# Optimization experiments

Measured on AMD Instinct MI355X. Metric: run time of the kernel, lower is better.

## Reference

```python
import jax, jax.numpy as jnp
import numpy as np

E = 800000
N_NODES = 25000
NUM_RADIAL = 6
HIDDEN = 256
OUT_EMB = 256
OUT_CH = 1
NUM_LAYERS = 3


def setup_inputs() -> dict:
    key = jax.random.key(0)
    ks = jax.random.split(key, 10)
    s = lambda fan_in: 1.0 / np.sqrt(fan_in)
    return {
        "x": jax.random.normal(ks[0], (E, HIDDEN), dtype=jnp.float32),
        "rbf": jax.random.normal(ks[1], (E, NUM_RADIAL), dtype=jnp.float32),
        "i": jax.random.randint(ks[2], (E,), 0, N_NODES, dtype=jnp.int64),
        "num_nodes": N_NODES,
        "W_rbf": jax.random.normal(ks[3], (HIDDEN, NUM_RADIAL), dtype=jnp.float32) * s(NUM_RADIAL),
        "W_up": jax.random.normal(ks[4], (OUT_EMB, HIDDEN), dtype=jnp.float32) * s(HIDDEN),
        "b_up": jnp.zeros((OUT_EMB,), dtype=jnp.float32),
        "Ws": jax.random.normal(ks[5], (NUM_LAYERS, OUT_EMB, OUT_EMB), dtype=jnp.float32) * s(OUT_EMB),
        "bs": jnp.zeros((NUM_LAYERS, OUT_EMB), dtype=jnp.float32),
        "W_out": jax.random.normal(ks[6], (OUT_CH, OUT_EMB), dtype=jnp.float32) * s(OUT_EMB),
    }


def reference(x, rbf, i, num_nodes, W_rbf, W_up, b_up, Ws, bs, W_out):
    # edge-wise: lin_rbf(rbf) * x  -> [E, hidden]
    h = jnp.einsum("er,hr->eh", rbf, W_rbf) * x
    # scatter-sum edges to nodes -> [N, hidden]
    h = jax.ops.segment_sum(h, i, num_segments=num_nodes)
    # lin_up (with bias) -> [N, out_emb]
    h = jnp.einsum("nh,oh->no", h, W_up) + b_up
    # MLP stack with swish activation
    for l in range(Ws.shape[0]):
        h = jax.nn.silu(jnp.einsum("no,po->np", h, Ws[l]) + bs[l])
    # final linear, no bias -> [N, out_channels]
    return jnp.einsum("no,co->nc", h, W_out)
```

## Files before the change

### kernel.cpp

```cpp
#include <hip/hip_runtime.h>
#include <stddef.h>

#define E_EDGES   800000
#define N_NODES   25000
#define NRADIAL   6
#define HIDDEN    256
#define OUT_EMB   256
#define NUM_LAYERS 3

__global__ void count_kernel(const int* __restrict__ idx, int* __restrict__ cnt) {
    int e = blockIdx.x * blockDim.x + threadIdx.x;
    if (e < E_EDGES) atomicAdd(&cnt[idx[e]], 1);
}

__global__ __launch_bounds__(1024) void scan_kernel(const int* __restrict__ cnt,
                                                    int* __restrict__ off,
                                                    int* __restrict__ cur) {
    __shared__ int warpsum[16];
    const int PER = 25;
    int t = threadIdx.x;
    int base = t * PER;
    int local[PER];
    int s = 0;
    #pragma unroll
    for (int j = 0; j < PER; ++j) {
        int n = base + j;
        int v = (n < N_NODES) ? cnt[n] : 0;
        local[j] = s;
        s += v;
    }
    int lane = t & 63, w = t >> 6;
    int incl = s;
    #pragma unroll
    for (int d = 1; d < 64; d <<= 1) {
        int y = __shfl_up(incl, d, 64);
        if (lane >= d) incl += y;
    }
    if (lane == 63) warpsum[w] = incl;
    __syncthreads();
    if (w == 0) {
        int v = (lane < 16) ? warpsum[lane] : 0;
        #pragma unroll
        for (int d = 1; d < 16; d <<= 1) {
            int y = __shfl_up(v, d, 64);
            if (lane >= d) v += y;
        }
        if (lane < 16) warpsum[lane] = v;
    }
    __syncthreads();
    int wbase = (w > 0) ? warpsum[w - 1] : 0;
    int texcl = wbase + (incl - s);
    #pragma unroll
    for (int j = 0; j < PER; ++j) {
        int n = base + j;
        if (n < N_NODES) { int o = texcl + local[j]; off[n] = o; cur[n] = o; }
    }
}

__global__ void fill_kernel(const int* __restrict__ idx, int* __restrict__ cur,
                            int* __restrict__ elist) {
    int e = blockIdx.x * blockDim.x + threadIdx.x;
    if (e < E_EDGES) {
        int n = idx[e];
        int pos = atomicAdd(&cur[n], 1);
        elist[pos] = e;
    }
}

__global__ __launch_bounds__(256) void gather_kernel(
        const float* __restrict__ x, const float* __restrict__ rbf,
        const float* __restrict__ W_rbf,
        const int* __restrict__ off, const int* __restrict__ cnt,
        const int* __restrict__ elist, float* __restrict__ node_h) {
    int wave = threadIdx.x >> 6;
    int lane = threadIdx.x & 63;
    int node = blockIdx.x * 4 + wave;
    if (node >= N_NODES) return;
    int c0 = lane * 4;

    float wr[4][NRADIAL];
    #pragma unroll
    for (int j = 0; j < 4; ++j)
        #pragma unroll
        for (int r = 0; r < NRADIAL; ++r)
            wr[j][r] = W_rbf[(c0 + j) * NRADIAL + r];

    float a0 = 0.f, a1 = 0.f, a2 = 0.f, a3 = 0.f;
    int start = off[node];
    int ne    = cnt[node];
    #pragma unroll 2
    for (int k = 0; k < ne; ++k) {
        int e = elist[start + k];
        const float2* r2 = reinterpret_cast<const float2*>(rbf + (size_t)e * NRADIAL);
        float2 ra = r2[0], rb = r2[1], rc = r2[2];
        float r0 = ra.x, r1 = ra.y, r2v = rb.x, r3 = rb.y, r4 = rc.x, r5 = rc.y;
        float4 xv = *reinterpret_cast<const float4*>(x + (size_t)e * HIDDEN + c0);
        float s0 = wr[0][0]*r0 + wr[0][1]*r1 + wr[0][2]*r2v + wr[0][3]*r3 + wr[0][4]*r4 + wr[0][5]*r5;
        float s1 = wr[1][0]*r0 + wr[1][1]*r1 + wr[1][2]*r2v + wr[1][3]*r3 + wr[1][4]*r4 + wr[1][5]*r5;
        float s2 = wr[2][0]*r0 + wr[2][1]*r1 + wr[2][2]*r2v + wr[2][3]*r3 + wr[2][4]*r4 + wr[2][5]*r5;
        float s3 = wr[3][0]*r0 + wr[3][1]*r1 + wr[3][2]*r2v + wr[3][3]*r3 + wr[3][4]*r4 + wr[3][5]*r5;
        a0 += s0 * xv.x; a1 += s1 * xv.y; a2 += s2 * xv.z; a3 += s3 * xv.w;
    }
    float4 o = make_float4(a0, a1, a2, a3);
    *reinterpret_cast<float4*>(node_h + (size_t)node * HIDDEN + c0) = o;
}

template<int DO_SILU>
__global__ __launch_bounds__(256) void gemm_kernel(
        const float* __restrict__ A,
        const float* __restrict__ W,
        const float* __restrict__ bias,
        float* __restrict__ C,
        int M) {
    constexpr int K  = 256;
    constexpr int BM = 128, BN = 64, BK = 16;
    __shared__ float As[BK][BM];
    __shared__ float Wsh[BK][BN];

    int tid  = threadIdx.x;
    int row0 = blockIdx.x * BM;
    int col0 = blockIdx.y * BN;
    int tx = tid & 15;
    int ty = tid >> 4;
    int tn  = tx * 4;
    int tm1 = ty * 4;
    int tm2 = 64 + ty * 4;

    float acc[2][4][4];
    #pragma unroll
    for (int mi = 0; mi < 2; ++mi)
        #pragma unroll
        for (int i = 0; i < 4; ++i)
            #pragma unroll
            for (int j = 0; j < 4; ++j) acc[mi][i][j] = 0.f;

    for (int kc = 0; kc < K; kc += BK) {
        #pragma unroll
        for (int l = 0; l < 2; ++l) {
            int id = tid * 2 + l;
            int r  = id >> 2;
            int kq = (id & 3) * 4;
            int grow = row0 + r;
            float4 v = make_float4(0.f, 0.f, 0.f, 0.f);
            if (grow < M)
                v = *reinterpret_cast<const float4*>(A + (size_t)grow * K + kc + kq);
            As[kq + 0][r] = v.x; As[kq + 1][r] = v.y;
            As[kq + 2][r] = v.z; As[kq + 3][r] = v.w;
        }
        {
            int r  = tid >> 2;
            int kq = (tid & 3) * 4;
            float4 v = *reinterpret_cast<const float4*>(W + (size_t)(col0 + r) * K + kc + kq);
            Wsh[kq + 0][r] = v.x; Wsh[kq + 1][r] = v.y;
            Wsh[kq + 2][r] = v.z; Wsh[kq + 3][r] = v.w;
        }
        __syncthreads();
        #pragma unroll
        for (int k = 0; k < BK; ++k) {
            float4 av1 = *reinterpret_cast<const float4*>(&As[k][tm1]);
            float4 av2 = *reinterpret_cast<const float4*>(&As[k][tm2]);
            float4 wv  = *reinterpret_cast<const float4*>(&Wsh[k][tn]);
            float a1v[4] = {av1.x, av1.y, av1.z, av1.w};
            float a2v[4] = {av2.x, av2.y, av2.z, av2.w};
            float wvv[4] = {wv.x, wv.y, wv.z, wv.w};
            #pragma unroll
            for (int i = 0; i < 4; ++i)
                #pragma unroll
                for (int j = 0; j < 4; ++j) {
                    acc[0][i][j] += a1v[i] * wvv[j];
                    acc[1][i][j] += a2v[i] * wvv[j];
                }
        }
        __syncthreads();
    }

    float4 bv = *reinterpret_cast<const float4*>(bias + col0 + tn);
    float bvv[4] = {bv.x, bv.y, bv.z, bv.w};
    #pragma unroll
    for (int mi = 0; mi < 2; ++mi) {
        int rbase = row0 + (mi ? tm2 : tm1);
        #pragma unroll
        for (int i = 0; i < 4; ++i) {
            int grow = rbase + i;
            if (grow < M) {
                float o[4];
                #pragma unroll
                for (int j = 0; j < 4; ++j) {
                    float v = acc[mi][i][j] + bvv[j];
                    if (DO_SILU) v = v / (1.f + expf(-v));
                    o[j] = v;
                }
                *reinterpret_cast<float4*>(C + (size_t)grow * 256 + col0 + tn) =
                    make_float4(o[0], o[1], o[2], o[3]);
            }
        }
    }
}

__global__ __launch_bounds__(256) void final_kernel(const float* __restrict__ H,
                                                    const float* __restrict__ Wout,
                                                    float* __restrict__ out, int M) {
    int wave = threadIdx.x >> 6, lane = threadIdx.x & 63;
    int row = blockIdx.x * 4 + wave;
    if (row >= M) return;
    float4 w = *reinterpret_cast<const float4*>(Wout + lane * 4);
    float4 h = *reinterpret_cast<const float4*>(H + (size_t)row * 256 + lane * 4);
    float s = h.x * w.x + h.y * w.y + h.z * w.z + h.w * w.w;
    #pragma unroll
    for (int d = 32; d > 0; d >>= 1) s += __shfl_down(s, d, 64);
    if (lane == 0) out[row] = s;
}

extern "C" void kernel_launch(void* const* d_in, const int* in_sizes, int n_in,
                              void* d_out, int out_size, void* d_ws, size_t ws_size,
                              hipStream_t stream) {
    const float* x     = (const float*)d_in[0];
    const float* rbf   = (const float*)d_in[1];
    const int*   idx   = (const int*)d_in[2];
    const float* W_rbf = (const float*)d_in[4];
    const float* W_up  = (const float*)d_in[5];
    const float* b_up  = (const float*)d_in[6];
    const float* Wl    = (const float*)d_in[7];
    const float* bl    = (const float*)d_in[8];
    const float* W_out = (const float*)d_in[9];
    float* out = (float*)d_out;

    char* ws = (char*)d_ws;
    const size_t SZ_CNT = 102400;
    const size_t SZ_EL  = (size_t)E_EDGES * 4;
    const size_t SZ_ACT = (size_t)N_NODES * 256 * 4;
    int*   cnt    = (int*)(ws);
    int*   off    = (int*)(ws + SZ_CNT);
    int*   cur    = (int*)(ws + 2 * SZ_CNT);
    int*   elist  = (int*)(ws + 3 * SZ_CNT);
    float* node_h = (float*)(ws + 3 * SZ_CNT + SZ_EL);
    float* bufA   = (float*)(ws + 3 * SZ_CNT + SZ_EL + SZ_ACT);
    float* bufB   = (float*)(ws + 3 * SZ_CNT + SZ_EL + 2 * SZ_ACT);

    hipMemsetAsync(cnt, 0, N_NODES * sizeof(int), stream);
    count_kernel<<<(E_EDGES + 255) / 256, 256, 0, stream>>>(idx, cnt);
    scan_kernel<<<1, 1024, 0, stream>>>(cnt, off, cur);
    fill_kernel<<<(E_EDGES + 255) / 256, 256, 0, stream>>>(idx, cur, elist);
    gather_kernel<<<N_NODES / 4, 256, 0, stream>>>(x, rbf, W_rbf, off, cnt, elist, node_h);

    dim3 gg((N_NODES + 127) / 128, 256 / 64);
    gemm_kernel<0><<<gg, 256, 0, stream>>>(node_h, W_up, b_up, bufA, N_NODES);
    gemm_kernel<1><<<gg, 256, 0, stream>>>(bufA, Wl + 0 * 65536, bl + 0,   bufB, N_NODES);
    gemm_kernel<1><<<gg, 256, 0, stream>>>(bufB, Wl + 1 * 65536, bl + 256, bufA, N_NODES);
    gemm_kernel<1><<<gg, 256, 0, stream>>>(bufA, Wl + 2 * 65536, bl + 512, bufB, N_NODES);
    final_kernel<<<(N_NODES + 3) / 4, 256, 0, stream>>>(bufB, W_out, out, N_NODES);
}
```

Measured before the change: 1.448 ms.

## Use split-bf16 MFMA GEMMs with async LDS staging for MLP layers

```diff
diff --git a/kernel.cpp b/kernel.cpp
--- a/kernel.cpp
+++ b/kernel.cpp
@@ -1,12 +1,34 @@
 #include <hip/hip_runtime.h>
 #include <stddef.h>
+#include <stdint.h>
 
 #define E_EDGES   800000
 #define N_NODES   25000
-#define NRADIAL   6
-#define HIDDEN    256
-#define OUT_EMB   256
-#define NUM_LAYERS 3
+#define MROWS_PAD 25088
+#define NBLK_M    196
+
+typedef __attribute__((ext_vector_type(8))) short frag8;
+typedef __attribute__((ext_vector_type(4))) float f32x4;
+
+__device__ __forceinline__ unsigned short f2b(float f) {
+    union { float f; unsigned int u; } c; c.f = f;
+    unsigned int u = c.u;
+    return (unsigned short)((u + 0x7fffu + ((u >> 16) & 1u)) >> 16);
+}
+__device__ __forceinline__ float b2f(unsigned short h) {
+    union { unsigned int u; float f; } c; c.u = ((unsigned int)h) << 16;
+    return c.f;
+}
+__device__ __forceinline__ void split2(float v, unsigned short& hi, unsigned short& lo) {
+    hi = f2b(v);
+    lo = f2b(v - b2f(hi));
+}
+
+__device__ __forceinline__ void gl_lds16(const void* g, void* l) {
+    __builtin_amdgcn_global_load_lds(
+        (const __attribute__((address_space(1))) unsigned int*)g,
+        (__attribute__((address_space(3))) unsigned int*)l, 16, 0, 0);
+}
 
 __global__ void count_kernel(const int* __restrict__ idx, int* __restrict__ cnt) {
     int e = blockIdx.x * blockDim.x + threadIdx.x;
@@ -61,151 +83,180 @@
                             int* __restrict__ elist) {
     int e = blockIdx.x * blockDim.x + threadIdx.x;
     if (e < E_EDGES) {
-        int n = idx[e];
-        int pos = atomicAdd(&cur[n], 1);
+        int pos = atomicAdd(&cur[idx[e]], 1);
         elist[pos] = e;
     }
+}
+
+__global__ void wconv_kernel(const float* __restrict__ Wup,
+                             const float* __restrict__ Wl,
+                             unsigned short* __restrict__ W2all) {
+    int t = blockIdx.x * blockDim.x + threadIdx.x;
+    if (t >= 4 * 65536) return;
+    int m = t >> 16, rem = t & 65535;
+    int o = rem >> 8, k = rem & 255;
+    float v = (m == 0) ? Wup[rem] : Wl[(m - 1) * 65536 + rem];
+    unsigned short hi, lo; split2(v, hi, lo);
+    unsigned short* row = W2all + (size_t)m * 131072 + (size_t)o * 512;
+    row[k] = hi; row[256 + k] = lo;
 }
 
 __global__ __launch_bounds__(256) void gather_kernel(
         const float* __restrict__ x, const float* __restrict__ rbf,
         const float* __restrict__ W_rbf,
         const int* __restrict__ off, const int* __restrict__ cnt,
-        const int* __restrict__ elist, float* __restrict__ node_h) {
+        const int* __restrict__ elist, unsigned short* __restrict__ H2) {
     int wave = threadIdx.x >> 6;
     int lane = threadIdx.x & 63;
     int node = blockIdx.x * 4 + wave;
     if (node >= N_NODES) return;
     int c0 = lane * 4;
 
-    float wr[4][NRADIAL];
+    float wr[4][6];
     #pragma unroll
     for (int j = 0; j < 4; ++j)
         #pragma unroll
-        for (int r = 0; r < NRADIAL; ++r)
-            wr[j][r] = W_rbf[(c0 + j) * NRADIAL + r];
+        for (int r = 0; r < 6; ++r)
+            wr[j][r] = W_rbf[(c0 + j) * 6 + r];
 
     float a0 = 0.f, a1 = 0.f, a2 = 0.f, a3 = 0.f;
     int start = off[node];
     int ne    = cnt[node];
-    #pragma unroll 2
-    for (int k = 0; k < ne; ++k) {
-        int e = elist[start + k];
-        const float2* r2 = reinterpret_cast<const float2*>(rbf + (size_t)e * NRADIAL);
-        float2 ra = r2[0], rb = r2[1], rc = r2[2];
-        float r0 = ra.x, r1 = ra.y, r2v = rb.x, r3 = rb.y, r4 = rc.x, r5 = rc.y;
-        float4 xv = *reinterpret_cast<const float4*>(x + (size_t)e * HIDDEN + c0);
-        float s0 = wr[0][0]*r0 + wr[0][1]*r1 + wr[0][2]*r2v + wr[0][3]*r3 + wr[0][4]*r4 + wr[0][5]*r5;
-        float s1 = wr[1][0]*r0 + wr[1][1]*r1 + wr[1][2]*r2v + wr[1][3]*r3 + wr[1][4]*r4 + wr[1][5]*r5;
-        float s2 = wr[2][0]*r0 + wr[2][1]*r1 + wr[2][2]*r2v + wr[2][3]*r3 + wr[2][4]*r4 + wr[2][5]*r5;
-        float s3 = wr[3][0]*r0 + wr[3][1]*r1 + wr[3][2]*r2v + wr[3][3]*r3 + wr[3][4]*r4 + wr[3][5]*r5;
-        a0 += s0 * xv.x; a1 += s1 * xv.y; a2 += s2 * xv.z; a3 += s3 * xv.w;
-    }
-    float4 o = make_float4(a0, a1, a2, a3);
-    *reinterpret_cast<float4*>(node_h + (size_t)node * HIDDEN + c0) = o;
+    for (int base = 0; base < ne; base += 64) {
+        int rem = ne - base;
+        int nb  = rem < 64 ? rem : 64;
+        int my_e = elist[start + base + (lane < rem ? lane : 0)];
+        #pragma unroll 2
+        for (int j = 0; j < nb; ++j) {
+            int e = __shfl(my_e, j, 64);
+            const float2* r2 = reinterpret_cast<const float2*>(rbf + (size_t)e * 6);
+            float2 ra = r2[0], rb = r2[1], rc = r2[2];
+            float4 xv = *reinterpret_cast<const float4*>(x + (size_t)e * 256 + c0);
+            float s0 = wr[0][0]*ra.x + wr[0][1]*ra.y + wr[0][2]*rb.x + wr[0][3]*rb.y + wr[0][4]*rc.x + wr[0][5]*rc.y;
+            float s1 = wr[1][0]*ra.x + wr[1][1]*ra.y + wr[1][2]*rb.x + wr[1][3]*rb.y + wr[1][4]*rc.x + wr[1][5]*rc.y;
+            float s2 = wr[2][0]*ra.x + wr[2][1]*ra.y + wr[2][2]*rb.x + wr[2][3]*rb.y + wr[2][4]*rc.x + wr[2][5]*rc.y;
+            float s3 = wr[3][0]*ra.x + wr[3][1]*ra.y + wr[3][2]*rb.x + wr[3][3]*rb.y + wr[3][4]*rc.x + wr[3][5]*rc.y;
+            a0 += s0 * xv.x; a1 += s1 * xv.y; a2 += s2 * xv.z; a3 += s3 * xv.w;
+        }
+    }
+    ushort4 hi4, lo4;
+    split2(a0, hi4.x, lo4.x);
+    split2(a1, hi4.y, lo4.y);
+    split2(a2, hi4.z, lo4.z);
+    split2(a3, hi4.w, lo4.w);
+    *reinterpret_cast<ushort4*>(H2 + (size_t)node * 512 + c0)       = hi4;
+    *reinterpret_cast<ushort4*>(H2 + (size_t)node * 512 + 256 + c0) = lo4;
 }
 
 template<int DO_SILU>
-__global__ __launch_bounds__(256) void gemm_kernel(
-        const float* __restrict__ A,
-        const float* __restrict__ W,
+__global__ __launch_bounds__(512, 1) void gemm_mfma(
+        const unsigned short* __restrict__ A2,
+        const unsigned short* __restrict__ W2,
         const float* __restrict__ bias,
-        float* __restrict__ C,
+        unsigned short* __restrict__ C2,
         int M) {
-    constexpr int K  = 256;
-    constexpr int BM = 128, BN = 64, BK = 16;
-    __shared__ float As[BK][BM];
-    __shared__ float Wsh[BK][BN];
-
+    constexpr int NST = 12;
+    __shared__ char lds[2][49152];
     int tid  = threadIdx.x;
-    int row0 = blockIdx.x * BM;
-    int col0 = blockIdx.y * BN;
-    int tx = tid & 15;
-    int ty = tid >> 4;
-    int tn  = tx * 4;
-    int tm1 = ty * 4;
-    int tm2 = 64 + ty * 4;
-
-    float acc[2][4][4];
-    #pragma unroll
-    for (int mi = 0; mi < 2; ++mi)
-        #pragma unroll
-        for (int i = 0; i < 4; ++i)
+    int row0 = blockIdx.x * 128;
+    int wid  = tid >> 6, lane = tid & 63;
+    int wm   = (wid >> 2) * 64;
+    int wn   = (wid & 3) * 64;
+    int fr   = lane & 15, fq = lane >> 4;
+
+    f32x4 acc[4][4];
+    #pragma unroll
+    for (int mi = 0; mi < 4; ++mi)
+        #pragma unroll
+        for (int nj = 0; nj < 4; ++nj)
+            acc[mi][nj] = (f32x4){0.f, 0.f, 0.f, 0.f};
+
+    auto stage = [&](int s, int b) {
+        int part = s >> 2, q = (s & 3) * 64;
+        int a_k0 = (part == 2 ? 256 : 0) + q;
+        int w_k0 = (part == 1 ? 256 : 0) + q;
+        #pragma unroll
+        for (int l = 0; l < 2; ++l) {
+            int chunk = l * 512 + tid;
+            int r = chunk >> 3, kc = chunk & 7;
+            int kcs = kc ^ (r & 7);
+            gl_lds16(A2 + (size_t)(row0 + r) * 512 + a_k0 + kcs * 8,
+                     &lds[b][chunk * 16]);
+        }
+        #pragma unroll
+        for (int l = 0; l < 4; ++l) {
+            int chunk = l * 512 + tid;
+            int r = chunk >> 3, kc = chunk & 7;
+            int kcs = kc ^ (r & 7);
+            gl_lds16(W2 + (size_t)r * 512 + w_k0 + kcs * 8,
+                     &lds[b][16384 + chunk * 16]);
+        }
+    };
+
+    stage(0, 0);
+    __syncthreads();
+    for (int s = 0; s < NST; ++s) {
+        if (s + 1 < NST) stage(s + 1, (s + 1) & 1);
+        const char* bufA = lds[s & 1];
+        const char* bufW = lds[s & 1] + 16384;
+        #pragma unroll
+        for (int ks = 0; ks < 2; ++ks) {
+            frag8 a[4], b[4];
             #pragma unroll
-            for (int j = 0; j < 4; ++j) acc[mi][i][j] = 0.f;
-
-    for (int kc = 0; kc < K; kc += BK) {
-        #pragma unroll
-        for (int l = 0; l < 2; ++l) {
-            int id = tid * 2 + l;
-            int r  = id >> 2;
-            int kq = (id & 3) * 4;
-            int grow = row0 + r;
-            float4 v = make_float4(0.f, 0.f, 0.f, 0.f);
-            if (grow < M)
-                v = *reinterpret_cast<const float4*>(A + (size_t)grow * K + kc + kq);
-            As[kq + 0][r] = v.x; As[kq + 1][r] = v.y;
-            As[kq + 2][r] = v.z; As[kq + 3][r] = v.w;
-        }
-        {
-            int r  = tid >> 2;
-            int kq = (tid & 3) * 4;
-            float4 v = *reinterpret_cast<const float4*>(W + (size_t)(col0 + r) * K + kc + kq);
-            Wsh[kq + 0][r] = v.x; Wsh[kq + 1][r] = v.y;
-            Wsh[kq + 2][r] = v.z; Wsh[kq + 3][r] = v.w;
+            for (int mi = 0; mi < 4; ++mi) {
+                int r  = wm + mi * 16 + fr;
+                int kc = ks * 4 + fq;
+                int kcs = kc ^ (r & 7);
+                a[mi] = *reinterpret_cast<const frag8*>(bufA + r * 128 + kcs * 16);
+            }
+            #pragma unroll
+            for (int nj = 0; nj < 4; ++nj) {
+                int r  = wn + nj * 16 + fr;
+                int kc = ks * 4 + fq;
+                int kcs = kc ^ (r & 7);
+                b[nj] = *reinterpret_cast<const frag8*>(bufW + r * 128 + kcs * 16);
+            }
+            #pragma unroll
+            for (int mi = 0; mi < 4; ++mi)
+                #pragma unroll
+                for (int nj = 0; nj < 4; ++nj)
+                    acc[mi][nj] = __builtin_amdgcn_mfma_f32_16x16x32_bf16(
+                        a[mi], b[nj], acc[mi][nj], 0, 0, 0);
         }
         __syncthreads();
-        #pragma unroll
-        for (int k = 0; k < BK; ++k) {
-            float4 av1 = *reinterpret_cast<const float4*>(&As[k][tm1]);
-            float4 av2 = *reinterpret_cast<const float4*>(&As[k][tm2]);
-            float4 wv  = *reinterpret_cast<const float4*>(&Wsh[k][tn]);
-            float a1v[4] = {av1.x, av1.y, av1.z, av1.w};
-            float a2v[4] = {av2.x, av2.y, av2.z, av2.w};
-            float wvv[4] = {wv.x, wv.y, wv.z, wv.w};
-            #pragma unroll
-            for (int i = 0; i < 4; ++i)
+    }
+
+    #pragma unroll
+    for (int mi = 0; mi < 4; ++mi) {
+        #pragma unroll
+        for (int r = 0; r < 4; ++r) {
+            int grow = row0 + wm + mi * 16 + fq * 4 + r;
+            if (grow < M) {
                 #pragma unroll
-                for (int j = 0; j < 4; ++j) {
-                    acc[0][i][j] += a1v[i] * wvv[j];
-                    acc[1][i][j] += a2v[i] * wvv[j];
+                for (int nj = 0; nj < 4; ++nj) {
+                    int col = wn + nj * 16 + fr;
+                    float v = acc[mi][nj][r] + bias[col];
+                    if (DO_SILU) v = v / (1.f + expf(-v));
+                    unsigned short hi, lo; split2(v, hi, lo);
+                    C2[(size_t)grow * 512 + col]       = hi;
+                    C2[(size_t)grow * 512 + 256 + col] = lo;
                 }
-        }
-        __syncthreads();
-    }
-
-    float4 bv = *reinterpret_cast<const float4*>(bias + col0 + tn);
-    float bvv[4] = {bv.x, bv.y, bv.z, bv.w};
-    #pragma unroll
-    for (int mi = 0; mi < 2; ++mi) {
-        int rbase = row0 + (mi ? tm2 : tm1);
-        #pragma unroll
-        for (int i = 0; i < 4; ++i) {
-            int grow = rbase + i;
-            if (grow < M) {
-                float o[4];
-                #pragma unroll
-                for (int j = 0; j < 4; ++j) {
-                    float v = acc[mi][i][j] + bvv[j];
-                    if (DO_SILU) v = v / (1.f + expf(-v));
-                    o[j] = v;
-                }
-                *reinterpret_cast<float4*>(C + (size_t)grow * 256 + col0 + tn) =
-                    make_float4(o[0], o[1], o[2], o[3]);
             }
         }
     }
 }
 
-__global__ __launch_bounds__(256) void final_kernel(const float* __restrict__ H,
+__global__ __launch_bounds__(256) void final_kernel(const unsigned short* __restrict__ H2,
                                                     const float* __restrict__ Wout,
                                                     float* __restrict__ out, int M) {
     int wave = threadIdx.x >> 6, lane = threadIdx.x & 63;
     int row = blockIdx.x * 4 + wave;
     if (row >= M) return;
     float4 w = *reinterpret_cast<const float4*>(Wout + lane * 4);
-    float4 h = *reinterpret_cast<const float4*>(H + (size_t)row * 256 + lane * 4);
-    float s = h.x * w.x + h.y * w.y + h.z * w.z + h.w * w.w;
+    ushort4 h = *reinterpret_cast<const ushort4*>(H2 + (size_t)row * 512 + lane * 4);
+    ushort4 l = *reinterpret_cast<const ushort4*>(H2 + (size_t)row * 512 + 256 + lane * 4);
+    float s = (b2f(h.x) + b2f(l.x)) * w.x + (b2f(h.y) + b2f(l.y)) * w.y +
+              (b2f(h.z) + b2f(l.z)) * w.z + (b2f(h.w) + b2f(l.w)) * w.w;
     #pragma unroll
     for (int d = 32; d > 0; d >>= 1) s += __shfl_down(s, d, 64);
     if (lane == 0) out[row] = s;
@@ -226,27 +277,25 @@
     float* out = (float*)d_out;
 
     char* ws = (char*)d_ws;
-    const size_t SZ_CNT = 102400;
-    const size_t SZ_EL  = (size_t)E_EDGES * 4;
-    const size_t SZ_ACT = (size_t)N_NODES * 256 * 4;
-    int*   cnt    = (int*)(ws);
-    int*   off    = (int*)(ws + SZ_CNT);
-    int*   cur    = (int*)(ws + 2 * SZ_CNT);
-    int*   elist  = (int*)(ws + 3 * SZ_CNT);
-    float* node_h = (float*)(ws + 3 * SZ_CNT + SZ_EL);
-    float* bufA   = (float*)(ws + 3 * SZ_CNT + SZ_EL + SZ_ACT);
-    float* bufB   = (float*)(ws + 3 * SZ_CNT + SZ_EL + 2 * SZ_ACT);
+    int*            cnt   = (int*)(ws);
+    int*            off   = (int*)(ws + 131072);
+    int*            cur   = (int*)(ws + 262144);
+    int*            elist = (int*)(ws + 393216);
+    unsigned short* W2all = (unsigned short*)(ws + 3670016);
+    unsigned short* H2    = (unsigned short*)(ws + 4718592);
+    unsigned short* bufA2 = (unsigned short*)(ws + 30408704);
+    unsigned short* bufB2 = (unsigned short*)(ws + 56098816);
 
     hipMemsetAsync(cnt, 0, N_NODES * sizeof(int), stream);
     count_kernel<<<(E_EDGES + 255) / 256, 256, 0, stream>>>(idx, cnt);
     scan_kernel<<<1, 1024, 0, stream>>>(cnt, off, cur);
     fill_kernel<<<(E_EDGES + 255) / 256, 256, 0, stream>>>(idx, cur, elist);
-    gather_kernel<<<N_NODES / 4, 256, 0, stream>>>(x, rbf, W_rbf, off, cnt, elist, node_h);
-
-    dim3 gg((N_NODES + 127) / 128, 256 / 64);
-    gemm_kernel<0><<<gg, 256, 0, stream>>>(node_h, W_up, b_up, bufA, N_NODES);
-    gemm_kernel<1><<<gg, 256, 0, stream>>>(bufA, Wl + 0 * 65536, bl + 0,   bufB, N_NODES);
-    gemm_kernel<1><<<gg, 256, 0, stream>>>(bufB, Wl + 1 * 65536, bl + 256, bufA, N_NODES);
-    gemm_kernel<1><<<gg, 256, 0, stream>>>(bufA, Wl + 2 * 65536, bl + 512, bufB, N_NODES);
-    final_kernel<<<(N_NODES + 3) / 4, 256, 0, stream>>>(bufB, W_out, out, N_NODES);
-}
+    wconv_kernel<<<1024, 256, 0, stream>>>(W_up, Wl, W2all);
+    gather_kernel<<<N_NODES / 4, 256, 0, stream>>>(x, rbf, W_rbf, off, cnt, elist, H2);
+
+    gemm_mfma<0><<<NBLK_M, 512, 0, stream>>>(H2,    W2all + 0 * 131072, b_up,     bufA2, N_NODES);
+    gemm_mfma<1><<<NBLK_M, 512, 0, stream>>>(bufA2, W2all + 1 * 131072, bl + 0,   bufB2, N_NODES);
+    gemm_mfma<1><<<NBLK_M, 512, 0, stream>>>(bufB2, W2all + 2 * 131072, bl + 256, bufA2, N_NODES);
+    gemm_mfma<1><<<NBLK_M, 512, 0, stream>>>(bufA2, W2all + 3 * 131072, bl + 512, bufB2, N_NODES);
+    final_kernel<<<(N_NODES + 3) / 4, 256, 0, stream>>>(bufB2, W_out, out, N_NODES);
+}
```

New measurement: 1.315 ms. 9.2% less time.
